# Performance work log

Hardware: AMD Instinct MI355X
Metric: run time of the kernel (lower is better)

## Reference

```python
import jax, jax.numpy as jnp
import numpy as np

B, S, I, H = 256, 1024, 1, 512


def setup_inputs() -> dict:
    key = jax.random.key(0)
    ks = jax.random.split(key, 12)
    s = 1.0 / np.sqrt(H)
    u = lambda k, shape: jax.random.uniform(k, shape, minval=-s, maxval=s, dtype=jnp.float32)
    return {
        "inputs": jax.random.normal(ks[0], (B, S, I), dtype=jnp.float32),
        "enc_Wih": u(ks[1], (4 * H, I)),
        "enc_Whh": u(ks[2], (4 * H, H)),
        "enc_bih": u(ks[3], (4 * H,)),
        "enc_bhh": u(ks[4], (4 * H,)),
        "dec_Wih": u(ks[5], (4 * H, I)),
        "dec_Whh": u(ks[6], (4 * H, H)),
        "dec_bih": u(ks[7], (4 * H,)),
        "dec_bhh": u(ks[8], (4 * H,)),
        "lin_W": u(ks[9], (I, H)),
        "lin_b": u(ks[10], (I,)),
        "target_len": 256,
    }


def _lstm_cell(x, h, c, Wih, Whh, bih, bhh):
    # x: [B, in], h/c: [B, H]. PyTorch gate order: i, f, g, o.
    gates = x @ Wih.T + h @ Whh.T + bih + bhh  # [B, 4H]
    i, f, g, o = jnp.split(gates, 4, axis=-1)
    c_new = jax.nn.sigmoid(f) * c + jax.nn.sigmoid(i) * jnp.tanh(g)
    h_new = jax.nn.sigmoid(o) * jnp.tanh(c_new)
    return h_new, c_new


def reference(inputs, enc_Wih, enc_Whh, enc_bih, enc_bhh,
              dec_Wih, dec_Whh, dec_bih, dec_bhh, lin_W, lin_b, target_len):
    bs = inputs.shape[0]
    dt = inputs.dtype
    h0 = jnp.zeros((bs, H), dt)
    c0 = jnp.zeros((bs, H), dt)

    # Encoder: scan over time; only final (h, c) is used downstream.
    def enc_step(carry, x_t):
        h, c = carry
        h, c = _lstm_cell(x_t, h, c, enc_Wih, enc_Whh, enc_bih, enc_bhh)
        return (h, c), None

    (h, c), _ = jax.lax.scan(enc_step, (h0, c0), jnp.swapaxes(inputs, 0, 1))

    def dec_step(carry, _):
        x, h, c = carry
        h, c = _lstm_cell(x, h, c, dec_Wih, dec_Whh, dec_bih, dec_bhh)
        out = h @ lin_W.T + lin_b  # [B, I]
        return (out, h, c), out

    x0 = inputs[:, -1, :]  # [B, I]
    _, outs = jax.lax.scan(dec_step, (x0, h, c), None, length=target_len)
    return jnp.swapaxes(outs, 0, 1)  # [B, target_len, I]
```

## Files before the change

kernel.cpp:

```cpp
#include <hip/hip_runtime.h>

#define B_    256
#define S_    1024
#define H_    512
#define G4_   2048
#define T_    256
#define NBLK  256
#define NTHR  1024
#define BB    16
#define NBG   16
#define LBN   16
#define HS2   260

typedef short bf8v  __attribute__((ext_vector_type(8)));
typedef float f4v   __attribute__((ext_vector_type(4)));
typedef int   i32x4 __attribute__((ext_vector_type(4)));

#define PERM_HI 0x07060302u
#define PERM_LO 0x05040100u

__global__ void fuse_dec_weights(const float* __restrict__ dec_Whh,
                                 const float* __restrict__ dec_Wih,
                                 const float* __restrict__ lin_W,
                                 float* __restrict__ W2)
{
    int idx = blockIdx.x * 256 + threadIdx.x;
    int j = idx >> 9, k = idx & 511;
    W2[idx] = fmaf(dec_Wih[j], lin_W[k], dec_Whh[idx]);
}

__device__ __forceinline__ float fsig(float x)
{
    return __builtin_amdgcn_rcpf(1.0f + __expf(-x));
}
__device__ __forceinline__ float ftanh(float x)
{
    return fmaf(-2.0f, __builtin_amdgcn_rcpf(1.0f + __expf(2.0f * x)), 1.0f);
}

__device__ __forceinline__ void bg_barrier(unsigned* arr, int ph)
{
    __syncthreads();
    if (threadIdx.x == 0) {
        unsigned prev = __hip_atomic_fetch_add(arr, 1u, __ATOMIC_RELAXED,
                                               __HIP_MEMORY_SCOPE_AGENT);
        const unsigned target = (unsigned)(ph + 1) * LBN;
        if (prev != target - 1u) {
            while (__hip_atomic_load(arr, __ATOMIC_RELAXED,
                                     __HIP_MEMORY_SCOPE_AGENT) < target)
                __builtin_amdgcn_s_sleep(1);
        }
    }
    __syncthreads();
}

__global__ void __launch_bounds__(NTHR)
seq2seq_kernel(const float* __restrict__ inputs,
               const float* __restrict__ enc_Wih,
               const float* __restrict__ enc_Whh,
               const float* __restrict__ enc_bih,
               const float* __restrict__ enc_bhh,
               const float* __restrict__ dec_Wih,
               const float* __restrict__ dec_bih,
               const float* __restrict__ dec_bhh,
               const float* __restrict__ lin_W,
               const float* __restrict__ lin_b,
               const float* __restrict__ W2,
               unsigned* __restrict__ hA0,
               unsigned* __restrict__ hB0,
               float* __restrict__ xcor,
               unsigned* __restrict__ bars,
               float* __restrict__ out)
{
    __shared__ unsigned hs_hi[BB * HS2];
    __shared__ unsigned hs_lo[BB * HS2];
    __shared__ float gbuf[4][128][BB + 1];

    const int tid  = threadIdx.x;
    const int w    = tid >> 6;
    const int lane = tid & 63;
    const int quad = lane >> 4;
    const int mn   = lane & 15;
    const int rs   = w & 3;
    const int ks   = w >> 2;
    const int bg   = blockIdx.x & (NBG - 1);
    const int lb   = blockIdx.x >> 4;
    const int bgbase = bg * BB;

    unsigned* arr = bars + bg * 64;

    i32x4 Ah[2][4], Al[2][4];
    auto loadA = [&](const float* __restrict__ W) {
        #pragma unroll
        for (int p = 0; p < 2; ++p) {
            const int jl = (rs * 2 + p) * 16 + mn;
            const int gate = jl >> 5, hsub = jl & 31;
            const float* rowp = W + (size_t)(gate * H_ + lb * 32 + hsub) * H_;
            #pragma unroll
            for (int l = 0; l < 4; ++l) {
                const float* rp = rowp + ks * 128 + l * 32 + quad * 8;
                float4 f0 = *(const float4*)rp;
                float4 f1 = *(const float4*)(rp + 4);
                unsigned b0 = __float_as_uint(f0.x), b1 = __float_as_uint(f0.y);
                unsigned b2 = __float_as_uint(f0.z), b3 = __float_as_uint(f0.w);
                unsigned b4 = __float_as_uint(f1.x), b5 = __float_as_uint(f1.y);
                unsigned b6 = __float_as_uint(f1.z), b7 = __float_as_uint(f1.w);
                i32x4 hi, lo;
                hi.x = __builtin_amdgcn_perm(b1, b0, PERM_HI);
                hi.y = __builtin_amdgcn_perm(b3, b2, PERM_HI);
                hi.z = __builtin_amdgcn_perm(b5, b4, PERM_HI);
                hi.w = __builtin_amdgcn_perm(b7, b6, PERM_HI);
                float r0 = f0.x - __uint_as_float(b0 & 0xffff0000u);
                float r1 = f0.y - __uint_as_float(b1 & 0xffff0000u);
                float r2 = f0.z - __uint_as_float(b2 & 0xffff0000u);
                float r3 = f0.w - __uint_as_float(b3 & 0xffff0000u);
                float r4 = f1.x - __uint_as_float(b4 & 0xffff0000u);
                float r5 = f1.y - __uint_as_float(b5 & 0xffff0000u);
                float r6 = f1.z - __uint_as_float(b6 & 0xffff0000u);
                float r7 = f1.w - __uint_as_float(b7 & 0xffff0000u);
                lo.x = __builtin_amdgcn_perm(__float_as_uint(r1), __float_as_uint(r0), PERM_HI);
                lo.y = __builtin_amdgcn_perm(__float_as_uint(r3), __float_as_uint(r2), PERM_HI);
                lo.z = __builtin_amdgcn_perm(__float_as_uint(r5), __float_as_uint(r4), PERM_HI);
                lo.w = __builtin_amdgcn_perm(__float_as_uint(r7), __float_as_uint(r6), PERM_HI);
                Ah[p][l] = hi; Al[p][l] = lo;
            }
        }
    };

    auto stage = [&](unsigned* hsrc) {
        unsigned long long* s = (unsigned long long*)hsrc;
        #pragma unroll
        for (int n = 0; n < 4; ++n) {
            const int iu = n * 1024 + tid;
            unsigned long long v = __hip_atomic_load(s + iu,
                                       __ATOMIC_RELAXED, __HIP_MEMORY_SCOPE_AGENT);
            const int row = iu >> 8, ku = iu & 255;
            unsigned vl = (unsigned)v, vh = (unsigned)(v >> 32);
            hs_hi[row * HS2 + ku] = __builtin_amdgcn_perm(vh, vl, PERM_HI);
            hs_lo[row * HS2 + ku] = __builtin_amdgcn_perm(vh, vl, PERM_LO);
        }
    };

    auto dots = [&]() {
        f4v acc0 = {0.f, 0.f, 0.f, 0.f};
        f4v acc1 = {0.f, 0.f, 0.f, 0.f};
        #pragma unroll
        for (int l = 0; l < 4; ++l) {
            const int boff = mn * HS2 + ks * 64 + l * 16 + quad * 4;
            i32x4 bhv = *(const i32x4*)(hs_hi + boff);
            i32x4 blv = *(const i32x4*)(hs_lo + boff);
            bf8v bh = __builtin_bit_cast(bf8v, bhv);
            bf8v bl = __builtin_bit_cast(bf8v, blv);
            bf8v a0h = __builtin_bit_cast(bf8v, Ah[0][l]);
            bf8v a0l = __builtin_bit_cast(bf8v, Al[0][l]);
            bf8v a1h = __builtin_bit_cast(bf8v, Ah[1][l]);
            bf8v a1l = __builtin_bit_cast(bf8v, Al[1][l]);
            acc0 = __builtin_amdgcn_mfma_f32_16x16x32_bf16(a0h, bh, acc0, 0, 0, 0);
            acc1 = __builtin_amdgcn_mfma_f32_16x16x32_bf16(a1h, bh, acc1, 0, 0, 0);
            acc0 = __builtin_amdgcn_mfma_f32_16x16x32_bf16(a0l, bh, acc0, 0, 0, 0);
            acc1 = __builtin_amdgcn_mfma_f32_16x16x32_bf16(a1l, bh, acc1, 0, 0, 0);
            acc0 = __builtin_amdgcn_mfma_f32_16x16x32_bf16(a0h, bl, acc0, 0, 0, 0);
            acc1 = __builtin_amdgcn_mfma_f32_16x16x32_bf16(a1h, bl, acc1, 0, 0, 0);
        }
        #pragma unroll
        for (int r = 0; r < 4; ++r) {
            gbuf[ks][(rs * 2 + 0) * 16 + quad * 4 + r][mn] = acc0[r];
            gbuf[ks][(rs * 2 + 1) * 16 + quad * 4 + r][mn] = acc1[r];
        }
    };

    auto proj = [&]() -> float {
        const unsigned* hh = hs_hi + w * HS2 + 4 * lane;
        const unsigned* hl = hs_lo + w * HS2 + 4 * lane;
        uint4 uh = *(const uint4*)hh;
        uint4 ul = *(const uint4*)hl;
        const float4* lwp = (const float4*)(lin_W + 8 * lane);
        float4 v0 = lwp[0], v1 = lwp[1];
        #define RL(h, l) (__uint_as_float((h) << 16) + __uint_as_float((l) << 16))
        #define RH(h, l) (__uint_as_float((h) & 0xffff0000u) + __uint_as_float((l) & 0xffff0000u))
        float s = RL(uh.x, ul.x) * v0.x + RH(uh.x, ul.x) * v0.y;
        s = fmaf(RL(uh.y, ul.y), v0.z, s); s = fmaf(RH(uh.y, ul.y), v0.w, s);
        s = fmaf(RL(uh.z, ul.z), v1.x, s); s = fmaf(RH(uh.z, ul.z), v1.y, s);
        s = fmaf(RL(uh.w, ul.w), v1.z, s); s = fmaf(RH(uh.w, ul.w), v1.w, s);
        #undef RL
        #undef RH
        s += __shfl_down(s, 32); s += __shfl_down(s, 16); s += __shfl_down(s, 8);
        s += __shfl_down(s, 4);  s += __shfl_down(s, 2);  s += __shfl_down(s, 1);
        return s;
    };

    const int hsubN = tid & 31, bN = tid >> 5;
    const int hidN  = lb * 32 + hsubN;
    const bool stateful = (tid < 512);

    const float ewi = enc_Wih[hidN],          ewf = enc_Wih[H_ + hidN];
    const float ewg = enc_Wih[2 * H_ + hidN], ewo = enc_Wih[3 * H_ + hidN];
    const float ebi = enc_bih[hidN] + enc_bhh[hidN];
    const float ebf = enc_bih[H_ + hidN] + enc_bhh[H_ + hidN];
    const float ebg = enc_bih[2 * H_ + hidN] + enc_bhh[2 * H_ + hidN];
    const float ebo = enc_bih[3 * H_ + hidN] + enc_bhh[3 * H_ + hidN];
    const float linb = lin_b[0];

    loadA(enc_Whh);

    if (stateful)
        __hip_atomic_store(&hA0[(size_t)(bgbase + bN) * H_ + hidN], 0u,
                           __ATOMIC_RELAXED, __HIP_MEMORY_SCOPE_AGENT);

    auto packh = [](float v) -> unsigned {
        unsigned hb = __float_as_uint(v) & 0xffff0000u;
        float r = v - __uint_as_float(hb);
        return hb | (__float_as_uint(r) >> 16);
    };

    auto gsum = [&](int row, int b) -> float {
        return (gbuf[0][row][b] + gbuf[1][row][b])
             + (gbuf[2][row][b] + gbuf[3][row][b]);
    };

    float cc = 0.f;
    unsigned* hcur = hA0;
    unsigned* hnxt = hB0;
    int ph = 0;

    #pragma unroll 1
    for (int t = 0; t < S_; ++t) {
        bg_barrier(arr, ph++);
        stage(hcur + (size_t)bgbase * H_);
        __syncthreads();
        dots();
        __syncthreads();
        if (stateful) {
            float xv = inputs[(size_t)(bgbase + bN) * S_ + t];
            float gi = gsum(hsubN, bN)      + fmaf(xv, ewi, ebi);
            float gf = gsum(32 + hsubN, bN) + fmaf(xv, ewf, ebf);
            float gg = gsum(64 + hsubN, bN) + fmaf(xv, ewg, ebg);
            float go = gsum(96 + hsubN, bN) + fmaf(xv, ewo, ebo);
            float i_ = fsig(gi), f_ = fsig(gf);
            float g_ = ftanh(gg), o_ = fsig(go);
            float cn = fmaf(f_, cc, i_ * g_);
            cc = cn;
            __hip_atomic_store(&hnxt[(size_t)(bgbase + bN) * H_ + hidN],
                               packh(o_ * ftanh(cn)),
                               __ATOMIC_RELAXED, __HIP_MEMORY_SCOPE_AGENT);
        }
        unsigned* tt = hcur; hcur = hnxt; hnxt = tt;
    }

    bg_barrier(arr, ph++);
    if (lb == 0) {
        stage(hcur + (size_t)bgbase * H_);
        __syncthreads();
        float s = proj();
        if (lane == 0) {
            float x0 = inputs[(size_t)(bgbase + w) * S_ + (S_ - 1)];
            __hip_atomic_store(&xcor[bgbase + w], x0 - (s + linb),
                               __ATOMIC_RELAXED, __HIP_MEMORY_SCOPE_AGENT);
        }
    }
    loadA(W2);
    const float dwi = dec_Wih[hidN],          dwf = dec_Wih[H_ + hidN];
    const float dwg = dec_Wih[2 * H_ + hidN], dwo = dec_Wih[3 * H_ + hidN];
    const float dbi = dec_bih[hidN] + dec_bhh[hidN] + dwi * linb;
    const float dbf = dec_bih[H_ + hidN] + dec_bhh[H_ + hidN] + dwf * linb;
    const float dbg = dec_bih[2 * H_ + hidN] + dec_bhh[2 * H_ + hidN] + dwg * linb;
    const float dbo = dec_bih[3 * H_ + hidN] + dec_bhh[3 * H_ + hidN] + dwo * linb;

    #pragma unroll 1
    for (int t = 0; t < T_; ++t) {
        bg_barrier(arr, ph++);
        stage(hcur + (size_t)bgbase * H_);
        __syncthreads();
        dots();
        if (lb == 0 && t > 0) {
            float s = proj();
            if (lane == 0)
                out[(size_t)(bgbase + w) * T_ + (t - 1)] = s + linb;
        }
        __syncthreads();
        if (stateful) {
            float gi = gsum(hsubN, bN)      + dbi;
            float gf = gsum(32 + hsubN, bN) + dbf;
            float gg = gsum(64 + hsubN, bN) + dbg;
            float go = gsum(96 + hsubN, bN) + dbo;
            if (t == 0) {
                float xc = __hip_atomic_load(&xcor[bgbase + bN],
                                             __ATOMIC_RELAXED, __HIP_MEMORY_SCOPE_AGENT);
                gi = fmaf(xc, dwi, gi); gf = fmaf(xc, dwf, gf);
                gg = fmaf(xc, dwg, gg); go = fmaf(xc, dwo, go);
            }
            float i_ = fsig(gi), f_ = fsig(gf);
            float g_ = ftanh(gg), o_ = fsig(go);
            float cn = fmaf(f_, cc, i_ * g_);
            cc = cn;
            __hip_atomic_store(&hnxt[(size_t)(bgbase + bN) * H_ + hidN],
                               packh(o_ * ftanh(cn)),
                               __ATOMIC_RELAXED, __HIP_MEMORY_SCOPE_AGENT);
        }
        unsigned* tt = hcur; hcur = hnxt; hnxt = tt;
    }

    bg_barrier(arr, ph++);
    if (lb == 0) {
        stage(hcur + (size_t)bgbase * H_);
        __syncthreads();
        float s = proj();
        if (lane == 0)
            out[(size_t)(bgbase + w) * T_ + (T_ - 1)] = s + linb;
    }
}

extern "C" void kernel_launch(void* const* d_in, const int* in_sizes, int n_in,
                              void* d_out, int out_size, void* d_ws, size_t ws_size,
                              hipStream_t stream)
{
    (void)in_sizes; (void)n_in; (void)out_size; (void)ws_size;

    const float* inputs  = (const float*)d_in[0];
    const float* enc_Wih = (const float*)d_in[1];
    const float* enc_Whh = (const float*)d_in[2];
    const float* enc_bih = (const float*)d_in[3];
    const float* enc_bhh = (const float*)d_in[4];
    const float* dec_Wih = (const float*)d_in[5];
    const float* dec_Whh = (const float*)d_in[6];
    const float* dec_bih = (const float*)d_in[7];
    const float* dec_bhh = (const float*)d_in[8];
    const float* lin_W   = (const float*)d_in[9];
    const float* lin_b   = (const float*)d_in[10];
    float* out = (float*)d_out;

    float* W2      = (float*)d_ws;
    unsigned* hA   = (unsigned*)(W2 + (size_t)G4_ * H_);
    unsigned* hB   = hA + (size_t)B_ * H_;
    float* xcor    = (float*)(hB + (size_t)B_ * H_);
    unsigned* bars = (unsigned*)(xcor + B_);

    hipMemsetAsync((void*)bars, 0, NBG * 64 * sizeof(unsigned), stream);

    hipLaunchKernelGGL(fuse_dec_weights, dim3((G4_ * H_) / 256), dim3(256), 0, stream,
                       dec_Whh, dec_Wih, lin_W, W2);

    void* args[] = {
        (void*)&inputs, (void*)&enc_Wih, (void*)&enc_Whh, (void*)&enc_bih, (void*)&enc_bhh,
        (void*)&dec_Wih, (void*)&dec_bih, (void*)&dec_bhh,
        (void*)&lin_W, (void*)&lin_b, (void*)&W2,
        (void*)&hA, (void*)&hB, (void*)&xcor, (void*)&bars, (void*)&out
    };
    hipLaunchCooperativeKernel((void*)seq2seq_kernel, dim3(NBLK), dim3(NTHR),
                               args, 0, stream);
}
```

Measured before the change: 4.047 ms.

## Split hidden state into hi/lo planes, DMA to LDS, reduce gates in-register

The hidden state is now stored in global memory as separate bf16 hi and lo planes, so staging becomes a direct global_load_lds DMA with no register unpacking. The weight row mapping is permuted so each lane's MFMA accumulator holds all four gates of two hidden units. One k-split wave group therefore does the cross-wave reduction and the LSTM update straight from registers, with fewer LDS writes and reads. Decoder biases are precomputed in the prep kernel. This adds a second global store per update and depends on the DMA write completing before the existing __syncthreads.

```diff
diff --git a/kernel.cpp b/kernel.cpp
--- a/kernel.cpp
+++ b/kernel.cpp
@@ -11,22 +11,31 @@
 #define NBG   16
 #define LBN   16
 #define HS2   260
+#define AUXC  0x11
 
 typedef short bf8v  __attribute__((ext_vector_type(8)));
 typedef float f4v   __attribute__((ext_vector_type(4)));
 typedef int   i32x4 __attribute__((ext_vector_type(4)));
 
+typedef const __attribute__((address_space(1))) void gas_void;
+typedef __attribute__((address_space(3))) void       las_void;
+
 #define PERM_HI 0x07060302u
-#define PERM_LO 0x05040100u
 
 __global__ void fuse_dec_weights(const float* __restrict__ dec_Whh,
                                  const float* __restrict__ dec_Wih,
                                  const float* __restrict__ lin_W,
-                                 float* __restrict__ W2)
+                                 const float* __restrict__ dec_bih,
+                                 const float* __restrict__ dec_bhh,
+                                 const float* __restrict__ lin_b,
+                                 float* __restrict__ W2,
+                                 float* __restrict__ dbias)
 {
     int idx = blockIdx.x * 256 + threadIdx.x;
     int j = idx >> 9, k = idx & 511;
     W2[idx] = fmaf(dec_Wih[j], lin_W[k], dec_Whh[idx]);
+    if (idx < G4_)
+        dbias[idx] = dec_bih[idx] + dec_bhh[idx] + dec_Wih[idx] * lin_b[0];
 }
 
 __device__ __forceinline__ float fsig(float x)
@@ -57,24 +66,23 @@
 __global__ void __launch_bounds__(NTHR)
 seq2seq_kernel(const float* __restrict__ inputs,
                const float* __restrict__ enc_Wih,
-               const float* __restrict__ enc_Whh,
                const float* __restrict__ enc_bih,
                const float* __restrict__ enc_bhh,
                const float* __restrict__ dec_Wih,
-               const float* __restrict__ dec_bih,
-               const float* __restrict__ dec_bhh,
                const float* __restrict__ lin_W,
                const float* __restrict__ lin_b,
+               const float* __restrict__ enc_Whh,
                const float* __restrict__ W2,
-               unsigned* __restrict__ hA0,
-               unsigned* __restrict__ hB0,
+               const float* __restrict__ dbias,
+               unsigned* __restrict__ hiA, unsigned* __restrict__ loA,
+               unsigned* __restrict__ hiB, unsigned* __restrict__ loB,
                float* __restrict__ xcor,
                unsigned* __restrict__ bars,
                float* __restrict__ out)
 {
     __shared__ unsigned hs_hi[BB * HS2];
     __shared__ unsigned hs_lo[BB * HS2];
-    __shared__ float gbuf[4][128][BB + 1];
+    __shared__ float gbuf[3 * 4 * 2 * 272];
 
     const int tid  = threadIdx.x;
     const int w    = tid >> 6;
@@ -86,6 +94,7 @@
     const int bg   = blockIdx.x & (NBG - 1);
     const int lb   = blockIdx.x >> 4;
     const int bgbase = bg * BB;
+    const bool leader = (ks == 3);
 
     unsigned* arr = bars + bg * 64;
 
@@ -93,12 +102,11 @@
     auto loadA = [&](const float* __restrict__ W) {
         #pragma unroll
         for (int p = 0; p < 2; ++p) {
-            const int jl = (rs * 2 + p) * 16 + mn;
-            const int gate = jl >> 5, hsub = jl & 31;
-            const float* rowp = W + (size_t)(gate * H_ + lb * 32 + hsub) * H_;
+            const int grow = (mn & 3) * H_ + lb * 32 + rs * 8 + 2 * (mn >> 2) + p;
+            const float* rowp = W + (size_t)grow * H_ + ks * 128 + quad * 8;
             #pragma unroll
             for (int l = 0; l < 4; ++l) {
-                const float* rp = rowp + ks * 128 + l * 32 + quad * 8;
+                const float* rp = rowp + l * 32;
                 float4 f0 = *(const float4*)rp;
                 float4 f1 = *(const float4*)(rp + 4);
                 unsigned b0 = __float_as_uint(f0.x), b1 = __float_as_uint(f0.y);
@@ -127,23 +135,17 @@
         }
     };
 
-    auto stage = [&](unsigned* hsrc) {
-        unsigned long long* s = (unsigned long long*)hsrc;
-        #pragma unroll
-        for (int n = 0; n < 4; ++n) {
-            const int iu = n * 1024 + tid;
-            unsigned long long v = __hip_atomic_load(s + iu,
-                                       __ATOMIC_RELAXED, __HIP_MEMORY_SCOPE_AGENT);
-            const int row = iu >> 8, ku = iu & 255;
-            unsigned vl = (unsigned)v, vh = (unsigned)(v >> 32);
-            hs_hi[row * HS2 + ku] = __builtin_amdgcn_perm(vh, vl, PERM_HI);
-            hs_lo[row * HS2 + ku] = __builtin_amdgcn_perm(vh, vl, PERM_LO);
-        }
-    };
-
-    auto dots = [&]() {
-        f4v acc0 = {0.f, 0.f, 0.f, 0.f};
-        f4v acc1 = {0.f, 0.f, 0.f, 0.f};
+    auto stage = [&](const unsigned* hi_src, const unsigned* lo_src) {
+        const size_t off = (size_t)(bgbase + w) * 256 + lane * 4;
+        __builtin_amdgcn_global_load_lds((gas_void*)(hi_src + off),
+                                         (las_void*)(hs_hi + w * HS2), 16, 0, AUXC);
+        __builtin_amdgcn_global_load_lds((gas_void*)(lo_src + off),
+                                         (las_void*)(hs_lo + w * HS2), 16, 0, AUXC);
+    };
+
+    auto dots = [&](f4v& acc0, f4v& acc1) {
+        acc0 = f4v{0.f, 0.f, 0.f, 0.f};
+        acc1 = f4v{0.f, 0.f, 0.f, 0.f};
         #pragma unroll
         for (int l = 0; l < 4; ++l) {
             const int boff = mn * HS2 + ks * 64 + l * 16 + quad * 4;
@@ -162,11 +164,44 @@
             acc0 = __builtin_amdgcn_mfma_f32_16x16x32_bf16(a0h, bl, acc0, 0, 0, 0);
             acc1 = __builtin_amdgcn_mfma_f32_16x16x32_bf16(a1h, bl, acc1, 0, 0, 0);
         }
-        #pragma unroll
-        for (int r = 0; r < 4; ++r) {
-            gbuf[ks][(rs * 2 + 0) * 16 + quad * 4 + r][mn] = acc0[r];
-            gbuf[ks][(rs * 2 + 1) * 16 + quad * 4 + r][mn] = acc1[r];
-        }
+    };
+
+    auto writegb = [&](f4v a0, f4v a1) {
+        float* gp = gbuf + ((ks * 4 + rs) * 2) * 272 + quad * 68 + mn * 4;
+        *(f4v*)gp = a0;
+        *(f4v*)(gp + 272) = a1;
+    };
+    auto reduceg = [&](f4v& a0, f4v& a1) {
+        const int gb = (rs * 2) * 272 + quad * 68 + mn * 4;
+        a0 += *(const f4v*)(gbuf + gb);
+        a0 += *(const f4v*)(gbuf + gb + 2176);
+        a0 += *(const f4v*)(gbuf + gb + 4352);
+        a1 += *(const f4v*)(gbuf + gb + 272);
+        a1 += *(const f4v*)(gbuf + gb + 272 + 2176);
+        a1 += *(const f4v*)(gbuf + gb + 272 + 4352);
+    };
+
+    auto lstm = [&](f4v g, float& cc) -> float {
+        float i_ = fsig(g[0]), f_ = fsig(g[1]);
+        float g_ = ftanh(g[2]), o_ = fsig(g[3]);
+        float cn = fmaf(f_, cc, i_ * g_);
+        cc = cn;
+        return o_ * ftanh(cn);
+    };
+
+    const int pidx = lb * 16 + rs * 4 + quad;
+    const int hid0 = lb * 32 + rs * 8 + 2 * quad;
+
+    auto storeh = [&](unsigned* hn, unsigned* ln, float h0, float h1) {
+        unsigned b0 = __float_as_uint(h0), b1 = __float_as_uint(h1);
+        unsigned hiw = __builtin_amdgcn_perm(b1, b0, PERM_HI);
+        float r0 = h0 - __uint_as_float(b0 & 0xffff0000u);
+        float r1 = h1 - __uint_as_float(b1 & 0xffff0000u);
+        unsigned low = __builtin_amdgcn_perm(__float_as_uint(r1),
+                                             __float_as_uint(r0), PERM_HI);
+        size_t pa = (size_t)(bgbase + mn) * 256 + pidx;
+        __hip_atomic_store(hn + pa, hiw, __ATOMIC_RELAXED, __HIP_MEMORY_SCOPE_AGENT);
+        __hip_atomic_store(ln + pa, low, __ATOMIC_RELAXED, __HIP_MEMORY_SCOPE_AGENT);
     };
 
     auto proj = [&]() -> float {
@@ -189,120 +224,118 @@
         return s;
     };
 
-    const int hsubN = tid & 31, bN = tid >> 5;
-    const int hidN  = lb * 32 + hsubN;
-    const bool stateful = (tid < 512);
-
-    const float ewi = enc_Wih[hidN],          ewf = enc_Wih[H_ + hidN];
-    const float ewg = enc_Wih[2 * H_ + hidN], ewo = enc_Wih[3 * H_ + hidN];
-    const float ebi = enc_bih[hidN] + enc_bhh[hidN];
-    const float ebf = enc_bih[H_ + hidN] + enc_bhh[H_ + hidN];
-    const float ebg = enc_bih[2 * H_ + hidN] + enc_bhh[2 * H_ + hidN];
-    const float ebo = enc_bih[3 * H_ + hidN] + enc_bhh[3 * H_ + hidN];
     const float linb = lin_b[0];
 
+    float encW[2][4], encB[2][4];
+    if (leader) {
+        #pragma unroll
+        for (int p = 0; p < 2; ++p)
+            #pragma unroll
+            for (int g4 = 0; g4 < 4; ++g4) {
+                const int j = g4 * H_ + hid0 + p;
+                encW[p][g4] = enc_Wih[j];
+                encB[p][g4] = enc_bih[j] + enc_bhh[j];
+            }
+    }
+
     loadA(enc_Whh);
 
-    if (stateful)
-        __hip_atomic_store(&hA0[(size_t)(bgbase + bN) * H_ + hidN], 0u,
-                           __ATOMIC_RELAXED, __HIP_MEMORY_SCOPE_AGENT);
-
-    auto packh = [](float v) -> unsigned {
-        unsigned hb = __float_as_uint(v) & 0xffff0000u;
-        float r = v - __uint_as_float(hb);
-        return hb | (__float_as_uint(r) >> 16);
-    };
-
-    auto gsum = [&](int row, int b) -> float {
-        return (gbuf[0][row][b] + gbuf[1][row][b])
-             + (gbuf[2][row][b] + gbuf[3][row][b]);
-    };
-
-    float cc = 0.f;
-    unsigned* hcur = hA0;
-    unsigned* hnxt = hB0;
+    if (leader) {
+        size_t pa = (size_t)(bgbase + mn) * 256 + pidx;
+        __hip_atomic_store(hiA + pa, 0u, __ATOMIC_RELAXED, __HIP_MEMORY_SCOPE_AGENT);
+        __hip_atomic_store(loA + pa, 0u, __ATOMIC_RELAXED, __HIP_MEMORY_SCOPE_AGENT);
+    }
+
+    float cc0 = 0.f, cc1 = 0.f;
+    unsigned *hic = hiA, *loc = loA, *hin = hiB, *lon = loB;
     int ph = 0;
 
     #pragma unroll 1
     for (int t = 0; t < S_; ++t) {
         bg_barrier(arr, ph++);
-        stage(hcur + (size_t)bgbase * H_);
-        __syncthreads();
-        dots();
-        __syncthreads();
-        if (stateful) {
-            float xv = inputs[(size_t)(bgbase + bN) * S_ + t];
-            float gi = gsum(hsubN, bN)      + fmaf(xv, ewi, ebi);
-            float gf = gsum(32 + hsubN, bN) + fmaf(xv, ewf, ebf);
-            float gg = gsum(64 + hsubN, bN) + fmaf(xv, ewg, ebg);
-            float go = gsum(96 + hsubN, bN) + fmaf(xv, ewo, ebo);
-            float i_ = fsig(gi), f_ = fsig(gf);
-            float g_ = ftanh(gg), o_ = fsig(go);
-            float cn = fmaf(f_, cc, i_ * g_);
-            cc = cn;
-            __hip_atomic_store(&hnxt[(size_t)(bgbase + bN) * H_ + hidN],
-                               packh(o_ * ftanh(cn)),
-                               __ATOMIC_RELAXED, __HIP_MEMORY_SCOPE_AGENT);
-        }
-        unsigned* tt = hcur; hcur = hnxt; hnxt = tt;
+        stage(hic, loc);
+        float xv = leader ? inputs[(size_t)(bgbase + mn) * S_ + t] : 0.f;
+        __syncthreads();
+        f4v acc0, acc1;
+        dots(acc0, acc1);
+        if (!leader) writegb(acc0, acc1);
+        __syncthreads();
+        if (leader) {
+            reduceg(acc0, acc1);
+            #pragma unroll
+            for (int g4 = 0; g4 < 4; ++g4) {
+                acc0[g4] += fmaf(xv, encW[0][g4], encB[0][g4]);
+                acc1[g4] += fmaf(xv, encW[1][g4], encB[1][g4]);
+            }
+            float h0 = lstm(acc0, cc0);
+            float h1 = lstm(acc1, cc1);
+            storeh(hin, lon, h0, h1);
+        }
+        unsigned* t1 = hic; hic = hin; hin = t1;
+        unsigned* t2 = loc; loc = lon; lon = t2;
     }
 
     bg_barrier(arr, ph++);
     if (lb == 0) {
-        stage(hcur + (size_t)bgbase * H_);
+        stage(hic, loc);
         __syncthreads();
         float s = proj();
         if (lane == 0) {
             float x0 = inputs[(size_t)(bgbase + w) * S_ + (S_ - 1)];
-            __hip_atomic_store(&xcor[bgbase + w], x0 - (s + linb),
+            __hip_atomic_store(&xcor[bgbase + w],
+                               __float_as_uint(0) * 0.f + (x0 - (s + linb)),
                                __ATOMIC_RELAXED, __HIP_MEMORY_SCOPE_AGENT);
         }
     }
     loadA(W2);
-    const float dwi = dec_Wih[hidN],          dwf = dec_Wih[H_ + hidN];
-    const float dwg = dec_Wih[2 * H_ + hidN], dwo = dec_Wih[3 * H_ + hidN];
-    const float dbi = dec_bih[hidN] + dec_bhh[hidN] + dwi * linb;
-    const float dbf = dec_bih[H_ + hidN] + dec_bhh[H_ + hidN] + dwf * linb;
-    const float dbg = dec_bih[2 * H_ + hidN] + dec_bhh[2 * H_ + hidN] + dwg * linb;
-    const float dbo = dec_bih[3 * H_ + hidN] + dec_bhh[3 * H_ + hidN] + dwo * linb;
 
     #pragma unroll 1
     for (int t = 0; t < T_; ++t) {
         bg_barrier(arr, ph++);
-        stage(hcur + (size_t)bgbase * H_);
-        __syncthreads();
-        dots();
+        stage(hic, loc);
+        f4v db0, db1;
+        if (leader) {
+            #pragma unroll
+            for (int g4 = 0; g4 < 4; ++g4) {
+                float2 d = *(const float2*)(dbias + g4 * H_ + hid0);
+                db0[g4] = d.x; db1[g4] = d.y;
+            }
+        }
+        __syncthreads();
+        f4v acc0, acc1;
+        dots(acc0, acc1);
+        if (!leader) writegb(acc0, acc1);
+        __syncthreads();
         if (lb == 0 && t > 0) {
             float s = proj();
             if (lane == 0)
                 out[(size_t)(bgbase + w) * T_ + (t - 1)] = s + linb;
         }
-        __syncthreads();
-        if (stateful) {
-            float gi = gsum(hsubN, bN)      + dbi;
-            float gf = gsum(32 + hsubN, bN) + dbf;
-            float gg = gsum(64 + hsubN, bN) + dbg;
-            float go = gsum(96 + hsubN, bN) + dbo;
+        if (leader) {
+            reduceg(acc0, acc1);
+            acc0 += db0;
+            acc1 += db1;
             if (t == 0) {
-                float xc = __hip_atomic_load(&xcor[bgbase + bN],
+                float xc = __hip_atomic_load(&xcor[bgbase + mn],
                                              __ATOMIC_RELAXED, __HIP_MEMORY_SCOPE_AGENT);
-                gi = fmaf(xc, dwi, gi); gf = fmaf(xc, dwf, gf);
-                gg = fmaf(xc, dwg, gg); go = fmaf(xc, dwo, go);
-            }
-            float i_ = fsig(gi), f_ = fsig(gf);
-            float g_ = ftanh(gg), o_ = fsig(go);
-            float cn = fmaf(f_, cc, i_ * g_);
-            cc = cn;
-            __hip_atomic_store(&hnxt[(size_t)(bgbase + bN) * H_ + hidN],
-                               packh(o_ * ftanh(cn)),
-                               __ATOMIC_RELAXED, __HIP_MEMORY_SCOPE_AGENT);
-        }
-        unsigned* tt = hcur; hcur = hnxt; hnxt = tt;
+                #pragma unroll
+                for (int g4 = 0; g4 < 4; ++g4) {
+                    float2 dw = *(const float2*)(dec_Wih + g4 * H_ + hid0);
+                    acc0[g4] = fmaf(xc, dw.x, acc0[g4]);
+                    acc1[g4] = fmaf(xc, dw.y, acc1[g4]);
+                }
+            }
+            float h0 = lstm(acc0, cc0);
+            float h1 = lstm(acc1, cc1);
+            storeh(hin, lon, h0, h1);
+        }
+        unsigned* t1 = hic; hic = hin; hin = t1;
+        unsigned* t2 = loc; loc = lon; lon = t2;
     }
 
     bg_barrier(arr, ph++);
     if (lb == 0) {
-        stage(hcur + (size_t)bgbase * H_);
+        stage(hic, loc);
         __syncthreads();
         float s = proj();
         if (lane == 0)
@@ -330,21 +363,25 @@
     float* out = (float*)d_out;
 
     float* W2      = (float*)d_ws;
-    unsigned* hA   = (unsigned*)(W2 + (size_t)G4_ * H_);
-    unsigned* hB   = hA + (size_t)B_ * H_;
-    float* xcor    = (float*)(hB + (size_t)B_ * H_);
+    float* dbias   = W2 + (size_t)G4_ * H_;
+    unsigned* hiA  = (unsigned*)(dbias + G4_);
+    unsigned* loA  = hiA + (size_t)B_ * 256;
+    unsigned* hiB  = loA + (size_t)B_ * 256;
+    unsigned* loB  = hiB + (size_t)B_ * 256;
+    float* xcor    = (float*)(loB + (size_t)B_ * 256);
     unsigned* bars = (unsigned*)(xcor + B_);
 
     hipMemsetAsync((void*)bars, 0, NBG * 64 * sizeof(unsigned), stream);
 
     hipLaunchKernelGGL(fuse_dec_weights, dim3((G4_ * H_) / 256), dim3(256), 0, stream,
-                       dec_Whh, dec_Wih, lin_W, W2);
+                       dec_Whh, dec_Wih, lin_W, dec_bih, dec_bhh, lin_b, W2, dbias);
 
     void* args[] = {
-        (void*)&inputs, (void*)&enc_Wih, (void*)&enc_Whh, (void*)&enc_bih, (void*)&enc_bhh,
-        (void*)&dec_Wih, (void*)&dec_bih, (void*)&dec_bhh,
-        (void*)&lin_W, (void*)&lin_b, (void*)&W2,
-        (void*)&hA, (void*)&hB, (void*)&xcor, (void*)&bars, (void*)&out
+        (void*)&inputs, (void*)&enc_Wih, (void*)&enc_bih, (void*)&enc_bhh,
+        (void*)&dec_Wih, (void*)&lin_W, (void*)&lin_b,
+        (void*)&enc_Whh, (void*)&W2, (void*)&dbias,
+        (void*)&hiA, (void*)&loA, (void*)&hiB, (void*)&loB,
+        (void*)&xcor, (void*)&bars, (void*)&out
     };
     hipLaunchCooperativeKernel((void*)seq2seq_kernel, dim3(NBLK), dim3(NTHR),
                                args, 0, stream);
```

After: 3.706 ms. 8.4% less time.
